# Performance work log

Hardware: AMD Instinct MI355X
Metric: run time of the kernel (lower is better)

The kernel has to match this reference:

```python
import jax, jax.numpy as jnp
import numpy as np

B, L, N = 2048, 64, 1024          # rows, lookback_period, nnodes
E, SE, F, NW, S = 32, 16, 8, 7, 20  # week emb, stop emb, n_features, nweekdays, stops per row
N_SHARED = E + F + SE             # 56; conv kernel width n_f = N_SHARED + 3 = 59


def setup_inputs() -> dict:
    key = jax.random.key(0)
    ks = jax.random.split(key, 12)
    return {
        "x": jax.random.normal(ks[0], (B, L, N), jnp.float32),
        "x_dist": jax.random.normal(ks[1], (N,), jnp.float32),
        "x_features": jax.random.normal(ks[2], (B, F), jnp.float32),
        "x_markov": jax.random.normal(ks[3], (B, N), jnp.float32),
        "stops": jax.random.randint(ks[4], (B, S), 0, N),
        "x_week": jax.random.randint(ks[5], (B,), 0, NW),
        "x_mask": jax.random.randint(ks[6], (B, N), 0, 2, jnp.int32),
        # learned parameters
        "stop_emb": jax.random.normal(ks[7], (N, SE), jnp.float32) * 0.1,
        "week_emb": jax.random.normal(ks[8], (NW, E), jnp.float32) * 0.1,
        "conv_w": jax.random.normal(ks[9], (N, N_SHARED + 3), jnp.float32) * 0.1,  # Conv1d weight [nnodes, 1, n_f] squeezed
        "conv_b": jax.random.normal(ks[10], (N,), jnp.float32) * 0.1,
        "fc1_w": jax.random.normal(ks[11], (L,), jnp.float32) * 0.1,  # Linear(L,1) weight
        "fc1_b": jnp.zeros((), jnp.float32),
    }


def reference(x, x_dist, x_features, x_markov, stops, x_week, x_mask,
              stop_emb, week_emb, conv_w, conv_b, fc1_w, fc1_b):
    # per-row sum of stop embeddings: [B, SE]
    x_embed = stop_emb[stops].sum(axis=1)
    # fc1 over lookback: out[b,n] = sum_l w[l] * x[b,l,n] + b   -> [B, N]
    out = jnp.einsum('bln,l->bn', x, fc1_w) + fc1_b
    # shared (node-independent) features, order matches torch concat: [week_emb, features, stop_emb_sum]
    shared = jnp.concatenate([week_emb[x_week], x_features, x_embed], axis=-1)  # [B, 56]
    # diagonal of strided Conv1d == per-node dot product with that node's kernel
    logits = (shared @ conv_w[:, :N_SHARED].T
              + out * conv_w[:, N_SHARED]
              + x_dist[None, :] * conv_w[:, N_SHARED + 1]
              + x_markov * conv_w[:, N_SHARED + 2]
              + conv_b)  # [B, N]
    logp = jax.nn.log_softmax(logits, axis=1)
    return jnp.where(x_mask.astype(bool), jnp.float32(-1e8), logp)
```

## Files before the change

kernel.cpp:

```cpp
#include <hip/hip_runtime.h>
#include <math.h>

#define BLOCK 256

__global__ __launch_bounds__(BLOCK, 2) void markov_fused(
    const float* __restrict__ x,
    const float* __restrict__ x_dist,
    const float* __restrict__ x_features,
    const float* __restrict__ x_markov,
    const int*   __restrict__ stops,
    const int*   __restrict__ x_week,
    const int*   __restrict__ x_mask,
    const float* __restrict__ stop_emb,
    const float* __restrict__ week_emb,
    const float* __restrict__ conv_w,
    const float* __restrict__ conv_b,
    const float* __restrict__ fc1_w,
    const float* __restrict__ fc1_b,
    float* __restrict__ out)
{
    constexpr int L = 64, N = 1024, E = 32, SE = 16, F = 8, S = 20;
    constexpr int NSH = 56;
    constexpr int NF  = 59;
    constexpr int NPT = N / BLOCK;
    constexpr int NWAVE = BLOCK / 64;

    __shared__ float sh_shared[NSH];
    __shared__ float sh_fc1[L];
    __shared__ float red_max[NWAVE];
    __shared__ float red_sum[NWAVE];

    const int b = blockIdx.x;
    const int t = threadIdx.x;

    if (t < L) sh_fc1[t] = fc1_w[t];
    if (t < E) {
        sh_shared[t] = week_emb[x_week[b] * E + t];
    } else if (t < E + F) {
        sh_shared[t] = x_features[b * F + (t - E)];
    } else if (t < NSH) {
        int j = t - (E + F);
        float s = 0.f;
        #pragma unroll
        for (int k = 0; k < S; ++k)
            s += stop_emb[stops[b * S + k] * SE + j];
        sh_shared[t] = s;
    }
    __syncthreads();

    const float4* xb = (const float4*)(x + (size_t)b * L * N);
    float4 acc = make_float4(0.f, 0.f, 0.f, 0.f);
    #pragma unroll 8
    for (int l = 0; l < L; ++l) {
        float  w = sh_fc1[l];
        float4 v = xb[l * (N / 4) + t];
        acc.x = fmaf(w, v.x, acc.x);
        acc.y = fmaf(w, v.y, acc.y);
        acc.z = fmaf(w, v.z, acc.z);
        acc.w = fmaf(w, v.w, acc.w);
    }
    const float bias = fc1_b[0];
    float o0 = acc.x + bias, o1 = acc.y + bias, o2 = acc.z + bias, o3 = acc.w + bias;

    float lg[NPT];
    float lmax = -INFINITY;
    const float* mkrow = x_markov + (size_t)b * N;
    #pragma unroll
    for (int i = 0; i < NPT; ++i) {
        const int n = 4 * t + i;
        const float* w = conv_w + (size_t)n * NF;
        float dot = 0.f;
        #pragma unroll
        for (int j = 0; j < NSH; ++j)
            dot = fmaf(sh_shared[j], w[j], dot);
        float o = (i == 0) ? o0 : (i == 1) ? o1 : (i == 2) ? o2 : o3;
        float v = dot
                + o          * w[NSH]
                + x_dist[n]  * w[NSH + 1]
                + mkrow[n]   * w[NSH + 2]
                + conv_b[n];
        lg[i] = v;
        lmax = fmaxf(lmax, v);
    }

    #pragma unroll
    for (int off = 32; off > 0; off >>= 1)
        lmax = fmaxf(lmax, __shfl_down(lmax, off, 64));
    if ((t & 63) == 0) red_max[t >> 6] = lmax;
    __syncthreads();
    float m = red_max[0];
    #pragma unroll
    for (int i = 1; i < NWAVE; ++i) m = fmaxf(m, red_max[i]);

    float se = 0.f;
    #pragma unroll
    for (int i = 0; i < NPT; ++i)
        se += expf(lg[i] - m);
    #pragma unroll
    for (int off = 32; off > 0; off >>= 1)
        se += __shfl_down(se, off, 64);
    if ((t & 63) == 0) red_sum[t >> 6] = se;
    __syncthreads();
    float Z = 0.f;
    #pragma unroll
    for (int i = 0; i < NWAVE; ++i) Z += red_sum[i];
    const float logZ = m + logf(Z);

    const int* mask = x_mask + (size_t)b * N;
    float4 res;
    res.x = mask[4 * t + 0] ? -1e8f : (lg[0] - logZ);
    res.y = mask[4 * t + 1] ? -1e8f : (lg[1] - logZ);
    res.z = mask[4 * t + 2] ? -1e8f : (lg[2] - logZ);
    res.w = mask[4 * t + 3] ? -1e8f : (lg[3] - logZ);
    ((float4*)(out + (size_t)b * N))[t] = res;
}

extern "C" void kernel_launch(void* const* d_in, const int* in_sizes, int n_in,
                              void* d_out, int out_size, void* d_ws, size_t ws_size,
                              hipStream_t stream) {
    const float* x          = (const float*)d_in[0];
    const float* x_dist     = (const float*)d_in[1];
    const float* x_features = (const float*)d_in[2];
    const float* x_markov   = (const float*)d_in[3];
    const int*   stops      = (const int*)  d_in[4];
    const int*   x_week     = (const int*)  d_in[5];
    const int*   x_mask     = (const int*)  d_in[6];
    const float* stop_emb   = (const float*)d_in[7];
    const float* week_emb   = (const float*)d_in[8];
    const float* conv_w     = (const float*)d_in[9];
    const float* conv_b     = (const float*)d_in[10];
    const float* fc1_w      = (const float*)d_in[11];
    const float* fc1_b      = (const float*)d_in[12];
    float* out = (float*)d_out;

    const int B = in_sizes[5];
    markov_fused<<<B, BLOCK, 0, stream>>>(
        x, x_dist, x_features, x_markov, stops, x_week, x_mask,
        stop_emb, week_emb, conv_w, conv_b, fc1_w, fc1_b, out);
}
```

Measured before the change: 775.6 us.

## Split static logits into tiled shared-memory GEMM kernel and slim main kernel

Moves the [B,56]x[56,N] embedding-weight product out of the per-row kernel into a separate tiled GEMM that stages both operands in LDS and writes a static logit matrix to workspace. The per-row kernel then only does the fc1 reduction over x plus elementwise combination, softmax and masking, with vectorised loads of the mask and packed weight columns. Before, every row block re-read strided conv_w rows per node; now the weights are reused across 64 rows per tile. The cost is four launches and an extra B*N float round trip through global memory.

```diff
diff --git a/kernel.cpp b/kernel.cpp
--- a/kernel.cpp
+++ b/kernel.cpp
@@ -3,29 +3,114 @@
 
 #define BLOCK 256
 
-__global__ __launch_bounds__(BLOCK, 2) void markov_fused(
+constexpr int L = 64, N = 1024, E = 32, SE = 16, F = 8, S = 20;
+constexpr int NSH = 56;
+constexpr int NF  = 59;
+
+__global__ void compute_shared(const float* __restrict__ x_features,
+                               const int*   __restrict__ stops,
+                               const int*   __restrict__ x_week,
+                               const float* __restrict__ stop_emb,
+                               const float* __restrict__ week_emb,
+                               float* __restrict__ sh_out)
+{
+    const int b = blockIdx.x;
+    const int t = threadIdx.x;
+    if (t < E) {
+        sh_out[b * NSH + t] = week_emb[x_week[b] * E + t];
+    } else if (t < E + F) {
+        sh_out[b * NSH + t] = x_features[b * F + (t - E)];
+    } else if (t < NSH) {
+        const int j = t - (E + F);
+        float s = 0.f;
+        #pragma unroll
+        for (int k = 0; k < S; ++k)
+            s += stop_emb[stops[b * S + k] * SE + j];
+        sh_out[b * NSH + t] = s;
+    }
+}
+
+__global__ void pack_w(const float* __restrict__ conv_w,
+                       const float* __restrict__ x_dist,
+                       const float* __restrict__ conv_b,
+                       float* __restrict__ w56,
+                       float* __restrict__ w58,
+                       float* __restrict__ colconst)
+{
+    const int n = blockIdx.x * blockDim.x + threadIdx.x;
+    if (n < N) {
+        const float* w = conv_w + (size_t)n * NF;
+        w56[n] = w[NSH];
+        w58[n] = w[NSH + 2];
+        colconst[n] = x_dist[n] * w[NSH + 1] + conv_b[n];
+    }
+}
+
+__global__ __launch_bounds__(BLOCK, 2) void gemm_static(
+    const float* __restrict__ shf,
+    const float* __restrict__ conv_w,
+    const float* __restrict__ colconst,
+    float* __restrict__ statc)
+{
+    __shared__ float Ash[64][NSH + 1];
+    __shared__ float Bsh[64][NSH + 1];
+
+    const int n0 = blockIdx.x * 64;
+    const int b0 = blockIdx.y * 64;
+    const int t  = threadIdx.x;
+
+    for (int idx = t; idx < 64 * NSH; idx += BLOCK) {
+        const int r = idx / NSH, c = idx % NSH;
+        Ash[r][c] = shf[(size_t)(b0 + r) * NSH + c];
+        Bsh[r][c] = conv_w[(size_t)(n0 + r) * NF + c];
+    }
+    __syncthreads();
+
+    const int tx = t & 15, ty = t >> 4;
+    float acc[4][4];
+    #pragma unroll
+    for (int i = 0; i < 4; ++i)
+        #pragma unroll
+        for (int k = 0; k < 4; ++k) acc[i][k] = 0.f;
+
+    #pragma unroll 8
+    for (int j = 0; j < NSH; ++j) {
+        float a[4], bb[4];
+        #pragma unroll
+        for (int i = 0; i < 4; ++i) a[i]  = Ash[ty * 4 + i][j];
+        #pragma unroll
+        for (int i = 0; i < 4; ++i) bb[i] = Bsh[tx * 4 + i][j];
+        #pragma unroll
+        for (int i = 0; i < 4; ++i)
+            #pragma unroll
+            for (int k = 0; k < 4; ++k)
+                acc[i][k] = fmaf(a[i], bb[k], acc[i][k]);
+    }
+
+    const float4 cc = *(const float4*)&colconst[n0 + tx * 4];
+    #pragma unroll
+    for (int i = 0; i < 4; ++i) {
+        float4 r;
+        r.x = acc[i][0] + cc.x;
+        r.y = acc[i][1] + cc.y;
+        r.z = acc[i][2] + cc.z;
+        r.w = acc[i][3] + cc.w;
+        *(float4*)&statc[(size_t)(b0 + ty * 4 + i) * N + n0 + tx * 4] = r;
+    }
+}
+
+__global__ __launch_bounds__(BLOCK, 4) void markov_main(
     const float* __restrict__ x,
-    const float* __restrict__ x_dist,
-    const float* __restrict__ x_features,
+    const float* __restrict__ statc,
+    const float* __restrict__ w56,
+    const float* __restrict__ w58,
     const float* __restrict__ x_markov,
-    const int*   __restrict__ stops,
-    const int*   __restrict__ x_week,
     const int*   __restrict__ x_mask,
-    const float* __restrict__ stop_emb,
-    const float* __restrict__ week_emb,
-    const float* __restrict__ conv_w,
-    const float* __restrict__ conv_b,
     const float* __restrict__ fc1_w,
     const float* __restrict__ fc1_b,
     float* __restrict__ out)
 {
-    constexpr int L = 64, N = 1024, E = 32, SE = 16, F = 8, S = 20;
-    constexpr int NSH = 56;
-    constexpr int NF  = 59;
-    constexpr int NPT = N / BLOCK;
     constexpr int NWAVE = BLOCK / 64;
-
-    __shared__ float sh_shared[NSH];
     __shared__ float sh_fc1[L];
     __shared__ float red_max[NWAVE];
     __shared__ float red_sum[NWAVE];
@@ -34,55 +119,33 @@
     const int t = threadIdx.x;
 
     if (t < L) sh_fc1[t] = fc1_w[t];
-    if (t < E) {
-        sh_shared[t] = week_emb[x_week[b] * E + t];
-    } else if (t < E + F) {
-        sh_shared[t] = x_features[b * F + (t - E)];
-    } else if (t < NSH) {
-        int j = t - (E + F);
-        float s = 0.f;
-        #pragma unroll
-        for (int k = 0; k < S; ++k)
-            s += stop_emb[stops[b * S + k] * SE + j];
-        sh_shared[t] = s;
-    }
     __syncthreads();
 
     const float4* xb = (const float4*)(x + (size_t)b * L * N);
     float4 acc = make_float4(0.f, 0.f, 0.f, 0.f);
-    #pragma unroll 8
+    #pragma unroll 16
     for (int l = 0; l < L; ++l) {
-        float  w = sh_fc1[l];
-        float4 v = xb[l * (N / 4) + t];
+        const float  w = sh_fc1[l];
+        const float4 v = xb[l * (N / 4) + t];
         acc.x = fmaf(w, v.x, acc.x);
         acc.y = fmaf(w, v.y, acc.y);
         acc.z = fmaf(w, v.z, acc.z);
         acc.w = fmaf(w, v.w, acc.w);
     }
     const float bias = fc1_b[0];
-    float o0 = acc.x + bias, o1 = acc.y + bias, o2 = acc.z + bias, o3 = acc.w + bias;
-
-    float lg[NPT];
-    float lmax = -INFINITY;
-    const float* mkrow = x_markov + (size_t)b * N;
-    #pragma unroll
-    for (int i = 0; i < NPT; ++i) {
-        const int n = 4 * t + i;
-        const float* w = conv_w + (size_t)n * NF;
-        float dot = 0.f;
-        #pragma unroll
-        for (int j = 0; j < NSH; ++j)
-            dot = fmaf(sh_shared[j], w[j], dot);
-        float o = (i == 0) ? o0 : (i == 1) ? o1 : (i == 2) ? o2 : o3;
-        float v = dot
-                + o          * w[NSH]
-                + x_dist[n]  * w[NSH + 1]
-                + mkrow[n]   * w[NSH + 2]
-                + conv_b[n];
-        lg[i] = v;
-        lmax = fmaxf(lmax, v);
-    }
-
+
+    const float4 st = ((const float4*)(statc + (size_t)b * N))[t];
+    const float4 wa = ((const float4*)w56)[t];
+    const float4 wc = ((const float4*)w58)[t];
+    const float4 mk = ((const float4*)(x_markov + (size_t)b * N))[t];
+
+    float lg[4];
+    lg[0] = st.x + (acc.x + bias) * wa.x + mk.x * wc.x;
+    lg[1] = st.y + (acc.y + bias) * wa.y + mk.y * wc.y;
+    lg[2] = st.z + (acc.z + bias) * wa.z + mk.z * wc.z;
+    lg[3] = st.w + (acc.w + bias) * wa.w + mk.w * wc.w;
+
+    float lmax = fmaxf(fmaxf(lg[0], lg[1]), fmaxf(lg[2], lg[3]));
     #pragma unroll
     for (int off = 32; off > 0; off >>= 1)
         lmax = fmaxf(lmax, __shfl_down(lmax, off, 64));
@@ -94,8 +157,7 @@
 
     float se = 0.f;
     #pragma unroll
-    for (int i = 0; i < NPT; ++i)
-        se += expf(lg[i] - m);
+    for (int i = 0; i < 4; ++i) se += expf(lg[i] - m);
     #pragma unroll
     for (int off = 32; off > 0; off >>= 1)
         se += __shfl_down(se, off, 64);
@@ -106,12 +168,12 @@
     for (int i = 0; i < NWAVE; ++i) Z += red_sum[i];
     const float logZ = m + logf(Z);
 
-    const int* mask = x_mask + (size_t)b * N;
+    const int4 mask = ((const int4*)(x_mask + (size_t)b * N))[t];
     float4 res;
-    res.x = mask[4 * t + 0] ? -1e8f : (lg[0] - logZ);
-    res.y = mask[4 * t + 1] ? -1e8f : (lg[1] - logZ);
-    res.z = mask[4 * t + 2] ? -1e8f : (lg[2] - logZ);
-    res.w = mask[4 * t + 3] ? -1e8f : (lg[3] - logZ);
+    res.x = mask.x ? -1e8f : (lg[0] - logZ);
+    res.y = mask.y ? -1e8f : (lg[1] - logZ);
+    res.z = mask.z ? -1e8f : (lg[2] - logZ);
+    res.w = mask.w ? -1e8f : (lg[3] - logZ);
     ((float4*)(out + (size_t)b * N))[t] = res;
 }
 
@@ -134,7 +196,20 @@
     float* out = (float*)d_out;
 
     const int B = in_sizes[5];
-    markov_fused<<<B, BLOCK, 0, stream>>>(
-        x, x_dist, x_features, x_markov, stops, x_week, x_mask,
-        stop_emb, week_emb, conv_w, conv_b, fc1_w, fc1_b, out);
-}
+
+    char* ws = (char*)d_ws;
+    float* sh_f     = (float*)(ws);
+    float* w56      = (float*)(ws + ((size_t)B * NSH * 4 + 255) / 256 * 256);
+    float* w58      = w56 + N;
+    float* colconst = w58 + N;
+    float* statc    = (float*)((char*)colconst + ((size_t)N * 4 + 255) / 256 * 256);
+
+    compute_shared<<<B, 64, 0, stream>>>(x_features, stops, x_week,
+                                         stop_emb, week_emb, sh_f);
+    pack_w<<<(N + 255) / 256, 256, 0, stream>>>(conv_w, x_dist, conv_b,
+                                                w56, w58, colconst);
+    dim3 ggrid(N / 64, B / 64);
+    gemm_static<<<ggrid, BLOCK, 0, stream>>>(sh_f, conv_w, colconst, statc);
+    markov_main<<<B, BLOCK, 0, stream>>>(x, statc, w56, w58, x_markov, x_mask,
+                                         fc1_w, fc1_b, out);
+}
```

Measured after the change: 724.2 us. -6.6%, faster.
